# Optimization experiments

Measured on AMD Instinct MI355X. Metric: run time of the kernel, lower is better.

Reference implementation:

```python
import jax, jax.numpy as jnp
import numpy as np

FEATURE_SIZE = 1000000  # padding index == FEATURE_SIZE
NEG_INF = -1e9


def _attn_pool(emb_table, hist_idx, ad_idx):
    # hist_idx: [B, L] int, ad_idx: [B] int
    hist = emb_table[hist_idx]          # [B, L, K] gather
    ad = emb_table[ad_idx]              # [B, K]
    score = jnp.einsum('blk,bk->bl', hist, ad)          # [B, L]
    score = jnp.where(hist_idx != FEATURE_SIZE, score, NEG_INF)
    w = jax.nn.softmax(score, axis=1)
    return jnp.einsum('blk,bl->bk', hist, w)            # [B, K]


def setup_inputs() -> dict:
    key = jax.random.key(0)
    ks = jax.random.split(key, 12)
    B, F, K = 4096, 8, 64
    V = FEATURE_SIZE + 1
    d_in = 3 * K + F * K  # 704
    inp = {
        'feature_idx': jax.random.randint(ks[0], (B, F), 0, FEATURE_SIZE),
        'hist_item': jax.random.randint(ks[1], (B, 350), 0, V),
        'hist_author': jax.random.randint(ks[2], (B, 250), 0, V),
        'hist_music': jax.random.randint(ks[3], (B, 100), 0, V),
        'emb_table': jax.random.normal(ks[4], (V, K), jnp.float32),
        'W1': jax.random.normal(ks[5], (d_in, 512), jnp.float32) * 0.02,
        'b1': jnp.zeros((512,), jnp.float32),
        'W2': jax.random.normal(ks[6], (512, 256), jnp.float32) * 0.02,
        'b2': jnp.zeros((256,), jnp.float32),
        'W3': jax.random.normal(ks[7], (256, 128), jnp.float32) * 0.02,
        'b3': jnp.zeros((128,), jnp.float32),
        'Wo': jax.random.normal(ks[8], (128, 1), jnp.float32) * 0.02,
        'bo': jnp.zeros((1,), jnp.float32),
    }
    return inp


def reference(feature_idx, hist_item, hist_author, hist_music, emb_table,
              W1, b1, W2, b2, W3, b3, Wo, bo):
    # ad indices for the three behavior features: columns 2, 3, 6
    pools = [
        _attn_pool(emb_table, hist_item, feature_idx[:, 2]),
        _attn_pool(emb_table, hist_author, feature_idx[:, 3]),
        _attn_pool(emb_table, hist_music, feature_idx[:, 6]),
    ]
    user_beha = jnp.concatenate(pools, axis=1)                    # [B, 3K]
    B = feature_idx.shape[0]
    ad_emb = emb_table[feature_idx].reshape(B, -1)                # [B, F*K]
    x = jnp.concatenate([user_beha, ad_emb], axis=1)              # [B, 704]
    x = jax.nn.relu(x @ W1 + b1)
    x = jax.nn.relu(x @ W2 + b2)
    x = jax.nn.relu(x @ W3 + b3)
    logits = x @ Wo + bo                                          # [B, 1]
    return logits
```

## Files before the change

### kernel.cpp

```cpp
#include <hip/hip_runtime.h>
#include <hip/hip_bf16.h>
#include <cstddef>

#define BATCH   4096
#define PAD_IDX 1000000
#define NEG_INF_F (-1e9f)

#define UPD(s, v)                                     \
    {                                                 \
        float nm = fmaxf(m, (s));                     \
        float sc = __expf(m - nm);                    \
        float e  = __expf((s) - nm);                  \
        d = fmaf(d, sc, e);                           \
        acc.x = fmaf(acc.x, sc, e * (v).x);           \
        acc.y = fmaf(acc.y, sc, e * (v).y);           \
        acc.z = fmaf(acc.z, sc, e * (v).z);           \
        acc.w = fmaf(acc.w, sc, e * (v).w);           \
        m = nm;                                       \
    }

#define MERGE(P)                                                  \
    {                                                             \
        float mo  = __shfl_xor(m, P);                             \
        float d_o = __shfl_xor(d, P);                             \
        float ax = __shfl_xor(acc.x, P);                          \
        float ay = __shfl_xor(acc.y, P);                          \
        float az = __shfl_xor(acc.z, P);                          \
        float aw = __shfl_xor(acc.w, P);                          \
        float nm = fmaxf(m, mo);                                  \
        float sA = __expf(m - nm), sB = __expf(mo - nm);          \
        d = d * sA + d_o * sB;                                    \
        acc.x = acc.x * sA + ax * sB;                             \
        acc.y = acc.y * sA + ay * sB;                             \
        acc.z = acc.z * sA + az * sB;                             \
        acc.w = acc.w * sA + aw * sB;                             \
        m = nm;                                                   \
    }

#define QRED(s)                       \
    s += __shfl_xor(s, 1);            \
    s += __shfl_xor(s, 2);            \
    s += __shfl_xor(s, 4);            \
    s += __shfl_xor(s, 8);

__global__ void __launch_bounds__(256) build_x_kernel(
    const int* __restrict__ fidx,
    const int* __restrict__ hist_item,
    const int* __restrict__ hist_author,
    const int* __restrict__ hist_music,
    const float* __restrict__ emb,
    float* __restrict__ x)
{
    const int w    = (blockIdx.x * 256 + threadIdx.x) >> 6;
    const int lane = threadIdx.x & 63;
    const int t16  = lane & 15;
    const int q    = lane >> 4;

    if (w < 3 * BATCH) {
        const int h = w >> 12;
        const int b = w & (BATCH - 1);
        int L, col, off;
        const int* hrow;
        if (h == 0)      { L = 350; col = 2; off = 0;   hrow = hist_item   + (size_t)b * 350; }
        else if (h == 1) { L = 250; col = 3; off = 64;  hrow = hist_author + (size_t)b * 250; }
        else             { L = 100; col = 6; off = 128; hrow = hist_music  + (size_t)b * 100; }

        const int ad_idx = fidx[b * 8 + col];
        const float4 ad4 = *(const float4*)(emb + (size_t)ad_idx * 64 + 4 * t16);

        float m = NEG_INF_F, d = 0.f;
        float4 acc = make_float4(0.f, 0.f, 0.f, 0.f);

        int l = 0;
        for (; l + 8 <= L; l += 8) {
            const int i0 = hrow[l + q];
            const int i1 = hrow[l + 4 + q];
            const float4 v0 = *(const float4*)(emb + (size_t)i0 * 64 + 4 * t16);
            const float4 v1 = *(const float4*)(emb + (size_t)i1 * 64 + 4 * t16);
            float s0 = v0.x * ad4.x + v0.y * ad4.y + v0.z * ad4.z + v0.w * ad4.w;
            float s1 = v1.x * ad4.x + v1.y * ad4.y + v1.z * ad4.z + v1.w * ad4.w;
            QRED(s0)
            QRED(s1)
            if (i0 == PAD_IDX) s0 = NEG_INF_F;
            if (i1 == PAD_IDX) s1 = NEG_INF_F;
            UPD(s0, v0)
            UPD(s1, v1)
        }
        for (; l < L; l += 4) {
            const int li = l + q;
            const int i0 = (li < L) ? hrow[li] : PAD_IDX;
            const float4 v0 = *(const float4*)(emb + (size_t)i0 * 64 + 4 * t16);
            float s0 = v0.x * ad4.x + v0.y * ad4.y + v0.z * ad4.z + v0.w * ad4.w;
            QRED(s0)
            if (i0 == PAD_IDX) s0 = NEG_INF_F;
            UPD(s0, v0)
        }

        MERGE(16)
        MERGE(32)

        if (lane < 16) {
            const float inv = 1.f / d;
            float4 r = make_float4(acc.x * inv, acc.y * inv, acc.z * inv, acc.w * inv);
            *(float4*)(x + (size_t)b * 704 + off + 4 * t16) = r;
        }
    } else {
        const int tt = w - 3 * BATCH;
        const int b  = tt >> 1;
        const int f  = ((tt & 1) << 2) + q;
        const int idx = fidx[b * 8 + f];
        const float4 v = *(const float4*)(emb + (size_t)idx * 64 + 4 * t16);
        *(float4*)(x + (size_t)b * 704 + 192 + (size_t)f * 64 + 4 * t16) = v;
    }
}

template <bool RELU>
__global__ void __launch_bounds__(256) gemm_bias(
    const float* __restrict__ A,
    const float* __restrict__ W,
    const float* __restrict__ bias,
    float* __restrict__ C,
    int M, int N, int K)
{
    __shared__ float As[16][68];
    __shared__ float Ws[16][64];

    const int tid = threadIdx.x;
    const int bm = blockIdx.y * 64;
    const int bn = blockIdx.x * 64;

    const int arow = tid >> 2;
    const int akq  = (tid & 3) << 2;
    const int wkk  = tid >> 4;
    const int wn   = (tid & 15) << 2;

    const int ty = tid >> 4, tx = tid & 15;
    const int m0 = ty << 2, n0 = tx << 2;

    float accm[4][4] = {};

    float4 a_reg = *(const float4*)(A + (size_t)(bm + arow) * K + akq);
    float4 w_reg = *(const float4*)(W + (size_t)wkk * N + bn + wn);

    for (int k0 = 0; k0 < K; k0 += 16) {
        As[akq + 0][arow] = a_reg.x;
        As[akq + 1][arow] = a_reg.y;
        As[akq + 2][arow] = a_reg.z;
        As[akq + 3][arow] = a_reg.w;
        *(float4*)&Ws[wkk][wn] = w_reg;
        __syncthreads();

        if (k0 + 16 < K) {
            a_reg = *(const float4*)(A + (size_t)(bm + arow) * K + (k0 + 16) + akq);
            w_reg = *(const float4*)(W + (size_t)(k0 + 16 + wkk) * N + bn + wn);
        }

#pragma unroll
        for (int kk = 0; kk < 16; ++kk) {
            const float4 av = *(const float4*)&As[kk][m0];
            const float4 bv = *(const float4*)&Ws[kk][n0];
            const float a[4] = {av.x, av.y, av.z, av.w};
            const float b[4] = {bv.x, bv.y, bv.z, bv.w};
#pragma unroll
            for (int i = 0; i < 4; ++i)
#pragma unroll
                for (int j = 0; j < 4; ++j)
                    accm[i][j] = fmaf(a[i], b[j], accm[i][j]);
        }
        __syncthreads();
    }

#pragma unroll
    for (int i = 0; i < 4; ++i) {
#pragma unroll
        for (int j = 0; j < 4; ++j) {
            float v = accm[i][j] + bias[bn + n0 + j];
            if (RELU) v = fmaxf(v, 0.f);
            C[(size_t)(bm + m0 + i) * N + bn + n0 + j] = v;
        }
    }
}

__global__ void __launch_bounds__(256) out_layer(
    const float* __restrict__ h3,
    const float* __restrict__ Wo,
    const float* __restrict__ bo,
    float* __restrict__ out, int M)
{
    const int w    = (blockIdx.x * 256 + threadIdx.x) >> 6;
    const int lane = threadIdx.x & 63;
    if (w >= M) return;
    float v = h3[(size_t)w * 128 + lane] * Wo[lane]
            + h3[(size_t)w * 128 + 64 + lane] * Wo[64 + lane];
    v += __shfl_xor(v, 32);
    v += __shfl_xor(v, 16);
    v += __shfl_xor(v, 8);
    v += __shfl_xor(v, 4);
    v += __shfl_xor(v, 2);
    v += __shfl_xor(v, 1);
    if (lane == 0) out[w] = v + bo[0];
}

extern "C" void kernel_launch(void* const* d_in, const int* in_sizes, int n_in,
                              void* d_out, int out_size, void* d_ws, size_t ws_size,
                              hipStream_t stream) {
    const int*   fidx  = (const int*)d_in[0];
    const int*   hitem = (const int*)d_in[1];
    const int*   hauth = (const int*)d_in[2];
    const int*   hmus  = (const int*)d_in[3];
    const float* emb   = (const float*)d_in[4];
    const float* W1 = (const float*)d_in[5];
    const float* b1 = (const float*)d_in[6];
    const float* W2 = (const float*)d_in[7];
    const float* b2 = (const float*)d_in[8];
    const float* W3 = (const float*)d_in[9];
    const float* b3 = (const float*)d_in[10];
    const float* Wo = (const float*)d_in[11];
    const float* bo = (const float*)d_in[12];
    float* out = (float*)d_out;

    float* x  = (float*)d_ws;
    float* h1 = x  + (size_t)BATCH * 704;
    float* h2 = h1 + (size_t)BATCH * 512;
    float* h3 = h2 + (size_t)BATCH * 256;

    build_x_kernel<<<5 * BATCH / 4, 256, 0, stream>>>(fidx, hitem, hauth, hmus, emb, x);

    gemm_bias<true><<<dim3(512 / 64, BATCH / 64), 256, 0, stream>>>(x,  W1, b1, h1, BATCH, 512, 704);
    gemm_bias<true><<<dim3(256 / 64, BATCH / 64), 256, 0, stream>>>(h1, W2, b2, h2, BATCH, 256, 512);
    gemm_bias<true><<<dim3(128 / 64, BATCH / 64), 256, 0, stream>>>(h2, W3, b3, h3, BATCH, 128, 256);

    out_layer<<<BATCH / 4, 256, 0, stream>>>(h3, Wo, bo, out, BATCH);
}
```

Measured before the change: 497.1 us.

## Switch MLP GEMMs to bf16 MFMA with bf16 activations and transposed weights

```diff
diff --git a/kernel.cpp b/kernel.cpp
--- a/kernel.cpp
+++ b/kernel.cpp
@@ -1,10 +1,22 @@
 #include <hip/hip_runtime.h>
-#include <hip/hip_bf16.h>
 #include <cstddef>
 
 #define BATCH   4096
 #define PAD_IDX 1000000
 #define NEG_INF_F (-1e9f)
+
+typedef __attribute__((ext_vector_type(8))) short bf16x8;
+typedef __attribute__((ext_vector_type(4))) float f32x4;
+typedef unsigned short u16;
+
+__device__ __forceinline__ u16 f2bf(float f) {
+    unsigned u = __float_as_uint(f);
+    return (u16)((u + 0x7fffu + ((u >> 16) & 1u)) >> 16);
+}
+__device__ __forceinline__ float bf2f(u16 b) {
+    return __uint_as_float(((unsigned)b) << 16);
+}
+
 
 #define UPD(s, v)                                     \
     {                                                 \
@@ -49,7 +61,7 @@
     const int* __restrict__ hist_author,
     const int* __restrict__ hist_music,
     const float* __restrict__ emb,
-    float* __restrict__ x)
+    u16* __restrict__ x)
 {
     const int w    = (blockIdx.x * 256 + threadIdx.x) >> 6;
     const int lane = threadIdx.x & 63;
@@ -101,8 +113,10 @@
 
         if (lane < 16) {
             const float inv = 1.f / d;
-            float4 r = make_float4(acc.x * inv, acc.y * inv, acc.z * inv, acc.w * inv);
-            *(float4*)(x + (size_t)b * 704 + off + 4 * t16) = r;
+            uint2 p;
+            p.x = (unsigned)f2bf(acc.x * inv) | ((unsigned)f2bf(acc.y * inv) << 16);
+            p.y = (unsigned)f2bf(acc.z * inv) | ((unsigned)f2bf(acc.w * inv) << 16);
+            *(uint2*)(x + (size_t)b * 704 + off + 4 * t16) = p;
         }
     } else {
         const int tt = w - 3 * BATCH;
@@ -110,79 +124,94 @@
         const int f  = ((tt & 1) << 2) + q;
         const int idx = fidx[b * 8 + f];
         const float4 v = *(const float4*)(emb + (size_t)idx * 64 + 4 * t16);
-        *(float4*)(x + (size_t)b * 704 + 192 + (size_t)f * 64 + 4 * t16) = v;
-    }
-}
-
-template <bool RELU>
-__global__ void __launch_bounds__(256) gemm_bias(
-    const float* __restrict__ A,
-    const float* __restrict__ W,
-    const float* __restrict__ bias,
-    float* __restrict__ C,
+        uint2 p;
+        p.x = (unsigned)f2bf(v.x) | ((unsigned)f2bf(v.y) << 16);
+        p.y = (unsigned)f2bf(v.z) | ((unsigned)f2bf(v.w) << 16);
+        *(uint2*)(x + (size_t)b * 704 + 192 + (size_t)f * 64 + 4 * t16) = p;
+    }
+}
+
+__global__ void __launch_bounds__(256) convert_weights(
+    const float* __restrict__ W1, const float* __restrict__ W2, const float* __restrict__ W3,
+    u16* __restrict__ W1T, u16* __restrict__ W2T, u16* __restrict__ W3T)
+{
+    int i = blockIdx.x * 256 + threadIdx.x;
+    if (i < 704 * 512) {
+        const int n = i / 704, k = i - n * 704;
+        W1T[i] = f2bf(W1[(size_t)k * 512 + n]);
+        return;
+    }
+    i -= 704 * 512;
+    if (i < 512 * 256) {
+        const int n = i / 512, k = i - n * 512;
+        W2T[i] = f2bf(W2[(size_t)k * 256 + n]);
+        return;
+    }
+    i -= 512 * 256;
+    if (i < 256 * 128) {
+        const int n = i / 256, k = i - n * 256;
+        W3T[i] = f2bf(W3[(size_t)k * 128 + n]);
+    }
+}
+
+template <int BN, bool RELU>
+__global__ void __launch_bounds__(256) gemm_mfma(
+    const u16* __restrict__ A, const u16* __restrict__ BT,
+    const float* __restrict__ bias, u16* __restrict__ C,
     int M, int N, int K)
 {
-    __shared__ float As[16][68];
-    __shared__ float Ws[16][64];
-
-    const int tid = threadIdx.x;
-    const int bm = blockIdx.y * 64;
-    const int bn = blockIdx.x * 64;
-
-    const int arow = tid >> 2;
-    const int akq  = (tid & 3) << 2;
-    const int wkk  = tid >> 4;
-    const int wn   = (tid & 15) << 2;
-
-    const int ty = tid >> 4, tx = tid & 15;
-    const int m0 = ty << 2, n0 = tx << 2;
-
-    float accm[4][4] = {};
-
-    float4 a_reg = *(const float4*)(A + (size_t)(bm + arow) * K + akq);
-    float4 w_reg = *(const float4*)(W + (size_t)wkk * N + bn + wn);
-
-    for (int k0 = 0; k0 < K; k0 += 16) {
-        As[akq + 0][arow] = a_reg.x;
-        As[akq + 1][arow] = a_reg.y;
-        As[akq + 2][arow] = a_reg.z;
-        As[akq + 3][arow] = a_reg.w;
-        *(float4*)&Ws[wkk][wn] = w_reg;
+    constexpr int NB = BN / 16;
+    __shared__ u16 As[64][40];
+    __shared__ u16 Bs[BN][40];
+
+    const int tid  = threadIdx.x;
+    const int wave = tid >> 6, lane = tid & 63;
+    const int quad = lane >> 4, l16 = lane & 15;
+    const int bm = blockIdx.y * 64, bn = blockIdx.x * BN;
+
+    const int srow = tid >> 2;
+    const int sk   = (tid & 3) * 8;
+
+    f32x4 acc[NB];
+#pragma unroll
+    for (int i = 0; i < NB; ++i) acc[i] = (f32x4){0.f, 0.f, 0.f, 0.f};
+
+    const size_t a_base = (size_t)(bm + srow) * K + sk;
+
+    for (int k0 = 0; k0 < K; k0 += 32) {
+        *(float4*)&As[srow][sk] = *(const float4*)(A + a_base + k0);
+#pragma unroll
+        for (int r0 = 0; r0 < BN; r0 += 64) {
+            *(float4*)&Bs[r0 + srow][sk] =
+                *(const float4*)(BT + (size_t)(bn + r0 + srow) * K + k0 + sk);
+        }
         __syncthreads();
 
-        if (k0 + 16 < K) {
-            a_reg = *(const float4*)(A + (size_t)(bm + arow) * K + (k0 + 16) + akq);
-            w_reg = *(const float4*)(W + (size_t)(k0 + 16 + wkk) * N + bn + wn);
-        }
-
-#pragma unroll
-        for (int kk = 0; kk < 16; ++kk) {
-            const float4 av = *(const float4*)&As[kk][m0];
-            const float4 bv = *(const float4*)&Ws[kk][n0];
-            const float a[4] = {av.x, av.y, av.z, av.w};
-            const float b[4] = {bv.x, bv.y, bv.z, bv.w};
-#pragma unroll
-            for (int i = 0; i < 4; ++i)
-#pragma unroll
-                for (int j = 0; j < 4; ++j)
-                    accm[i][j] = fmaf(a[i], b[j], accm[i][j]);
+        const bf16x8 af = *(const bf16x8*)&As[wave * 16 + l16][quad * 8];
+#pragma unroll
+        for (int ni = 0; ni < NB; ++ni) {
+            const bf16x8 bf = *(const bf16x8*)&Bs[ni * 16 + l16][quad * 8];
+            acc[ni] = __builtin_amdgcn_mfma_f32_16x16x32_bf16(af, bf, acc[ni], 0, 0, 0);
         }
         __syncthreads();
     }
 
 #pragma unroll
-    for (int i = 0; i < 4; ++i) {
-#pragma unroll
-        for (int j = 0; j < 4; ++j) {
-            float v = accm[i][j] + bias[bn + n0 + j];
+    for (int ni = 0; ni < NB; ++ni) {
+        const int col = bn + ni * 16 + l16;
+        const float bv = bias[col];
+#pragma unroll
+        for (int r = 0; r < 4; ++r) {
+            const int row = bm + wave * 16 + quad * 4 + r;
+            float v = acc[ni][r] + bv;
             if (RELU) v = fmaxf(v, 0.f);
-            C[(size_t)(bm + m0 + i) * N + bn + n0 + j] = v;
+            C[(size_t)row * N + col] = f2bf(v);
         }
     }
 }
 
 __global__ void __launch_bounds__(256) out_layer(
-    const float* __restrict__ h3,
+    const u16* __restrict__ h3,
     const float* __restrict__ Wo,
     const float* __restrict__ bo,
     float* __restrict__ out, int M)
@@ -190,8 +219,8 @@
     const int w    = (blockIdx.x * 256 + threadIdx.x) >> 6;
     const int lane = threadIdx.x & 63;
     if (w >= M) return;
-    float v = h3[(size_t)w * 128 + lane] * Wo[lane]
-            + h3[(size_t)w * 128 + 64 + lane] * Wo[64 + lane];
+    float v = bf2f(h3[(size_t)w * 128 + lane]) * Wo[lane]
+            + bf2f(h3[(size_t)w * 128 + 64 + lane]) * Wo[64 + lane];
     v += __shfl_xor(v, 32);
     v += __shfl_xor(v, 16);
     v += __shfl_xor(v, 8);
@@ -219,16 +248,25 @@
     const float* bo = (const float*)d_in[12];
     float* out = (float*)d_out;
 
-    float* x  = (float*)d_ws;
-    float* h1 = x  + (size_t)BATCH * 704;
-    float* h2 = h1 + (size_t)BATCH * 512;
-    float* h3 = h2 + (size_t)BATCH * 256;
+    u16* x   = (u16*)d_ws;
+    u16* h1  = x   + (size_t)BATCH * 704;
+    u16* h2  = h1  + (size_t)BATCH * 512;
+    u16* h3  = h2  + (size_t)BATCH * 256;
+    u16* w1t = h3  + (size_t)BATCH * 128;
+    u16* w2t = w1t + (size_t)704 * 512;
+    u16* w3t = w2t + (size_t)512 * 256;
+
+    convert_weights<<<(704 * 512 + 512 * 256 + 256 * 128) / 256, 256, 0, stream>>>(
+        W1, W2, W3, w1t, w2t, w3t);
 
     build_x_kernel<<<5 * BATCH / 4, 256, 0, stream>>>(fidx, hitem, hauth, hmus, emb, x);
 
-    gemm_bias<true><<<dim3(512 / 64, BATCH / 64), 256, 0, stream>>>(x,  W1, b1, h1, BATCH, 512, 704);
-    gemm_bias<true><<<dim3(256 / 64, BATCH / 64), 256, 0, stream>>>(h1, W2, b2, h2, BATCH, 256, 512);
-    gemm_bias<true><<<dim3(128 / 64, BATCH / 64), 256, 0, stream>>>(h2, W3, b3, h3, BATCH, 128, 256);
+    gemm_mfma<128, true><<<dim3(512 / 128, BATCH / 64), 256, 0, stream>>>(
+        x, w1t, b1, h1, BATCH, 512, 704);
+    gemm_mfma<64, true><<<dim3(256 / 64, BATCH / 64), 256, 0, stream>>>(
+        h1, w2t, b2, h2, BATCH, 256, 512);
+    gemm_mfma<64, true><<<dim3(128 / 64, BATCH / 64), 256, 0, stream>>>(
+        h2, w3t, b3, h3, BATCH, 128, 256);
 
     out_layer<<<BATCH / 4, 256, 0, stream>>>(h3, Wo, bo, out, BATCH);
 }
```

Result: faster. 450.4 us (-9.4%).
